# Kernel tuning notes

Hardware: AMD Instinct MI355X
Metric: run time of the kernel (lower is better)

Reference implementation:

```python
import jax, jax.numpy as jnp
import numpy as np

N_NODES = 50000
N_EDGES = 800000
D_IN, H, D_OUT = 128, 128, 64


def setup_inputs() -> dict:
    key = jax.random.key(0)
    ks = jax.random.split(key, 8)
    x = jax.random.normal(ks[0], (N_NODES, D_IN), dtype=jnp.float32)
    edge_index = jax.random.randint(ks[1], (2, N_EDGES), 0, N_NODES, dtype=jnp.int64)
    s = 0.05
    return {
        "x": x,
        "edge_index": edge_index,
        # PyG Linear weights are [out, in]; y = x @ W.T + b
        "W_rel1": jax.random.normal(ks[2], (H, D_IN), dtype=jnp.float32) * s,
        "W_root1": jax.random.normal(ks[3], (H, D_IN), dtype=jnp.float32) * s,
        "b1": jax.random.normal(ks[4], (H,), dtype=jnp.float32) * s,
        "W_rel2": jax.random.normal(ks[5], (D_OUT, H), dtype=jnp.float32) * s,
        "W_root2": jax.random.normal(ks[6], (D_OUT, H), dtype=jnp.float32) * s,
        "b2": jax.random.normal(ks[7], (D_OUT,), dtype=jnp.float32) * s,
    }


def graph_conv(x, src, dst, W_rel, W_root, b):
    # sum-aggregate raw neighbor features, then apply linear (equivalent to
    # transforming each message first, but cheaper: one gather + one GEMM).
    agg = jax.ops.segment_sum(x[src], dst, num_segments=N_NODES)  # [N, D]
    return jnp.einsum('nd,hd->nh', agg, W_rel) \
         + jnp.einsum('nd,hd->nh', x, W_root) + b


def reference(x, edge_index, W_rel1, W_root1, b1, W_rel2, W_root2, b2):
    src, dst = edge_index[0], edge_index[1]  # messages flow src -> dst
    t = jax.nn.relu(graph_conv(x, src, dst, W_rel1, W_root1, b1))
    t = graph_conv(t, src, dst, W_rel2, W_root2, b2)
    return t
```

## Files before the change

kernel.cpp:

```cpp
#include <hip/hip_runtime.h>

#define NNODES 50000
#define DIM 128
#define SCAN_CHUNK 4096
#define NSCAN 13
#define PREP_BLOCKS 3200
#define POISON ((int)0xAAAAAAAA)

typedef __attribute__((ext_vector_type(8))) __bf16 bf16x8;
typedef __attribute__((ext_vector_type(4))) float f32x4;

__device__ inline unsigned short f2b(float f) {
    unsigned int u = __float_as_uint(f);
    u += 0x7fffu + ((u >> 16) & 1u);
    return (unsigned short)(u >> 16);
}
__device__ inline float blo(unsigned int u) { return __uint_as_float(u << 16); }
__device__ inline float bhi(unsigned int u) { return __uint_as_float(u & 0xffff0000u); }
__device__ inline unsigned int pack2(float a, float b) {
    return (unsigned int)f2b(a) | ((unsigned int)f2b(b) << 16);
}

__global__ __launch_bounds__(256) void k_prep(
    const float* __restrict__ x, unsigned short* __restrict__ xb, int n4,
    const float* __restrict__ Wa1, const float* __restrict__ Wb1,
    const float* __restrict__ Wa2, const float* __restrict__ Wb2,
    unsigned short* __restrict__ wa1, unsigned short* __restrict__ wb1,
    unsigned short* __restrict__ wa2, unsigned short* __restrict__ wb2,
    const int* __restrict__ dst, int* __restrict__ counts,
    int* __restrict__ rank, int n_edges)
{
    const int gid = blockIdx.x * 256 + threadIdx.x;

    const int i1 = blockIdx.x * 512 + threadIdx.x;
    const int i2 = i1 + 256;
    const bool ok1 = i1 < n4, ok2 = i2 < n4;
    float4 v1, v2;
    if (ok1) v1 = reinterpret_cast<const float4*>(x)[i1];
    if (ok2) v2 = reinterpret_cast<const float4*>(x)[i2];

    if (gid < n_edges) rank[gid] = atomicAdd(&counts[dst[gid]], 1);

    if (gid < 16384) { wa1[gid] = f2b(Wa1[gid]); wb1[gid] = f2b(Wb1[gid]); }
    if (gid < 8192)  { wa2[gid] = f2b(Wa2[gid]); wb2[gid] = f2b(Wb2[gid]); }

    if (ok1) {
        uint2 o;
        o.x = pack2(v1.x, v1.y);
        o.y = pack2(v1.z, v1.w);
        reinterpret_cast<uint2*>(xb)[i1] = o;
    }
    if (ok2) {
        uint2 o;
        o.x = pack2(v2.x, v2.y);
        o.y = pack2(v2.z, v2.w);
        reinterpret_cast<uint2*>(xb)[i2] = o;
    }
}

__global__ __launch_bounds__(1024) void k_scan_local(
    const int* __restrict__ counts, int* __restrict__ rowptr,
    int* __restrict__ bsum, int n)
{
    __shared__ int wsum[16];
    const int lane = threadIdx.x & 63;
    const int wid = threadIdx.x >> 6;
    int i = blockIdx.x * SCAN_CHUNK + threadIdx.x * 4;
    int4 v = make_int4(0, 0, 0, 0);
    if (i + 3 < n) {
        v = *reinterpret_cast<const int4*>(counts + i);
        v.x -= POISON; v.y -= POISON; v.z -= POISON; v.w -= POISON;
    } else {
        if (i + 0 < n) v.x = counts[i + 0] - POISON;
        if (i + 1 < n) v.y = counts[i + 1] - POISON;
        if (i + 2 < n) v.z = counts[i + 2] - POISON;
    }
    int tot = v.x + v.y + v.z + v.w;
    int s = tot;
#pragma unroll
    for (int off = 1; off < 64; off <<= 1) {
        int t = __shfl_up(s, off);
        if (lane >= off) s += t;
    }
    if (lane == 63) wsum[wid] = s;
    __syncthreads();
    if (wid == 0 && lane < 16) {
        int ws = wsum[lane];
#pragma unroll
        for (int off = 1; off < 16; off <<= 1) {
            int t = __shfl_up(ws, off);
            if (lane >= off) ws += t;
        }
        wsum[lane] = ws;
    }
    __syncthreads();
    int prefix = ((wid > 0) ? wsum[wid - 1] : 0) + (s - tot);
    int4 o;
    o.x = prefix;
    o.y = prefix + v.x;
    o.z = o.y + v.y;
    o.w = o.z + v.z;
    if (i + 3 <= n) {
        *reinterpret_cast<int4*>(rowptr + i) = o;
    } else {
        if (i + 0 <= n) rowptr[i + 0] = o.x;
        if (i + 1 <= n) rowptr[i + 1] = o.y;
        if (i + 2 <= n) rowptr[i + 2] = o.z;
    }
    if (threadIdx.x == 1023) bsum[blockIdx.x] = wsum[15];
}

__device__ inline void build_prefix_lds(const int* __restrict__ bsum, int* pre) {
    if (threadIdx.x < 16) {
        int off = 0;
#pragma unroll 1
        for (int j = 0; j < NSCAN && j < (int)threadIdx.x; ++j) off += bsum[j];
        pre[threadIdx.x] = off;
    }
    __syncthreads();
}

__global__ __launch_bounds__(256) void k_place(
    const int* __restrict__ src, const int* __restrict__ dst,
    const int* __restrict__ rank, const int* __restrict__ rowptr,
    const int* __restrict__ bsum, int* __restrict__ srcs_sorted, int n_edges)
{
    __shared__ int pre[16];
    build_prefix_lds(bsum, pre);
    int e = (blockIdx.x * 256 + threadIdx.x) * 8;
    if (e + 7 < n_edges) {
        int4 s4a = *reinterpret_cast<const int4*>(src + e);
        int4 s4b = *reinterpret_cast<const int4*>(src + e + 4);
        int4 d4a = *reinterpret_cast<const int4*>(dst + e);
        int4 d4b = *reinterpret_cast<const int4*>(dst + e + 4);
        int4 r4a = *reinterpret_cast<const int4*>(rank + e);
        int4 r4b = *reinterpret_cast<const int4*>(rank + e + 4);
        srcs_sorted[rowptr[d4a.x] + pre[d4a.x >> 12] + r4a.x - POISON] = s4a.x;
        srcs_sorted[rowptr[d4a.y] + pre[d4a.y >> 12] + r4a.y - POISON] = s4a.y;
        srcs_sorted[rowptr[d4a.z] + pre[d4a.z >> 12] + r4a.z - POISON] = s4a.z;
        srcs_sorted[rowptr[d4a.w] + pre[d4a.w >> 12] + r4a.w - POISON] = s4a.w;
        srcs_sorted[rowptr[d4b.x] + pre[d4b.x >> 12] + r4b.x - POISON] = s4b.x;
        srcs_sorted[rowptr[d4b.y] + pre[d4b.y >> 12] + r4b.y - POISON] = s4b.y;
        srcs_sorted[rowptr[d4b.z] + pre[d4b.z >> 12] + r4b.z - POISON] = s4b.z;
        srcs_sorted[rowptr[d4b.w] + pre[d4b.w >> 12] + r4b.w - POISON] = s4b.w;
    } else {
        for (; e < n_edges; ++e) {
            int d = dst[e];
            srcs_sorted[rowptr[d] + pre[d >> 12] + rank[e] - POISON] = src[e];
        }
    }
}

__global__ __launch_bounds__(256) void k_gather_sum(
    const unsigned short* __restrict__ xb, const int* __restrict__ rowptr,
    const int* __restrict__ bsum, const int* __restrict__ srcs,
    unsigned short* __restrict__ aggb)
{
    __shared__ int pre[16];
    build_prefix_lds(bsum, pre);
    int node = blockIdx.x * 16 + (threadIdx.x >> 4);
    if (node >= NNODES) return;
    int seg = threadIdx.x & 15;
    int beg = rowptr[node] + pre[node >> 12];
    int end = rowptr[node + 1] + pre[(node + 1) >> 12];
    float acc[8];
#pragma unroll
    for (int i = 0; i < 8; ++i) acc[i] = 0.f;
    int e = beg;
#pragma unroll 1
    for (; e + 7 < end; e += 8) {
        uint4 v[8];
#pragma unroll
        for (int u = 0; u < 8; ++u) {
            int s = srcs[e + u];
            v[u] = *reinterpret_cast<const uint4*>(xb + (size_t)s * DIM + seg * 8);
        }
#pragma unroll
        for (int u = 0; u < 8; ++u) {
            acc[0] += blo(v[u].x); acc[1] += bhi(v[u].x);
            acc[2] += blo(v[u].y); acc[3] += bhi(v[u].y);
            acc[4] += blo(v[u].z); acc[5] += bhi(v[u].z);
            acc[6] += blo(v[u].w); acc[7] += bhi(v[u].w);
        }
    }
#pragma unroll 1
    for (; e + 1 < end; e += 2) {
        int s0 = srcs[e], s1 = srcs[e + 1];
        uint4 v0 = *reinterpret_cast<const uint4*>(xb + (size_t)s0 * DIM + seg * 8);
        uint4 v1 = *reinterpret_cast<const uint4*>(xb + (size_t)s1 * DIM + seg * 8);
        acc[0] += blo(v0.x) + blo(v1.x); acc[1] += bhi(v0.x) + bhi(v1.x);
        acc[2] += blo(v0.y) + blo(v1.y); acc[3] += bhi(v0.y) + bhi(v1.y);
        acc[4] += blo(v0.z) + blo(v1.z); acc[5] += bhi(v0.z) + bhi(v1.z);
        acc[6] += blo(v0.w) + blo(v1.w); acc[7] += bhi(v0.w) + bhi(v1.w);
    }
    if (e < end) {
        int s0 = srcs[e];
        uint4 v = *reinterpret_cast<const uint4*>(xb + (size_t)s0 * DIM + seg * 8);
        acc[0] += blo(v.x); acc[1] += bhi(v.x);
        acc[2] += blo(v.y); acc[3] += bhi(v.y);
        acc[4] += blo(v.z); acc[5] += bhi(v.z);
        acc[6] += blo(v.w); acc[7] += bhi(v.w);
    }
    uint4 o;
    o.x = pack2(acc[0], acc[1]);
    o.y = pack2(acc[2], acc[3]);
    o.z = pack2(acc[4], acc[5]);
    o.w = pack2(acc[6], acc[7]);
    *reinterpret_cast<uint4*>(aggb + (size_t)node * DIM + seg * 8) = o;
}

template <int BN, bool RELU, bool OUTBF16>
__global__ __launch_bounds__(256) void k_gemm_direct(
    const unsigned short* __restrict__ Ab,
    const unsigned short* __restrict__ Bb,
    const unsigned short* __restrict__ Wa,
    const unsigned short* __restrict__ Wb,
    const float* __restrict__ bias, void* __restrict__ Cout, int n_nodes)
{
    constexpr int NT = BN / 16;
    const int tid = threadIdx.x;
    const int wave = tid >> 6;
    const int lane = tid & 63;
    const int quad = lane >> 4;
    const int l16 = lane & 15;
    const int n0 = blockIdx.x * 64;
    const int arow = n0 + wave * 16 + l16;
    const bool ok = arow < n_nodes;

    f32x4 acc[NT];
#pragma unroll
    for (int nt = 0; nt < NT; ++nt) {
        f32x4 z = {0.f, 0.f, 0.f, 0.f};
        acc[nt] = z;
    }

#pragma unroll 1
    for (int kk = 0; kk < 4; ++kk) {
        const unsigned short* __restrict__ Asrc = (kk < 2) ? Ab : Bb;
        const unsigned short* __restrict__ Wsrc = (kk < 2) ? Wa : Wb;
        const int ko = (kk & 1) * 64;
        bf16x8 a0 = {}, a1 = {};
        if (ok) {
            a0 = *reinterpret_cast<const bf16x8*>(
                Asrc + (size_t)arow * DIM + ko + quad * 8);
            a1 = *reinterpret_cast<const bf16x8*>(
                Asrc + (size_t)arow * DIM + ko + 32 + quad * 8);
        }
#pragma unroll
        for (int nt = 0; nt < NT; ++nt) {
            bf16x8 b = *reinterpret_cast<const bf16x8*>(
                Wsrc + (size_t)(nt * 16 + l16) * DIM + ko + quad * 8);
            acc[nt] = __builtin_amdgcn_mfma_f32_16x16x32_bf16(a0, b, acc[nt], 0, 0, 0);
        }
#pragma unroll
        for (int nt = 0; nt < NT; ++nt) {
            bf16x8 b = *reinterpret_cast<const bf16x8*>(
                Wsrc + (size_t)(nt * 16 + l16) * DIM + ko + 32 + quad * 8);
            acc[nt] = __builtin_amdgcn_mfma_f32_16x16x32_bf16(a1, b, acc[nt], 0, 0, 0);
        }
    }

#pragma unroll
    for (int nt = 0; nt < NT; ++nt) {
        int col = nt * 16 + l16;
        float bv = bias[col];
#pragma unroll
        for (int reg = 0; reg < 4; ++reg) {
            int row = n0 + wave * 16 + quad * 4 + reg;
            if (row >= n_nodes) continue;
            float v = acc[nt][reg] + bv;
            if (RELU) v = fmaxf(v, 0.f);
            if (OUTBF16)
                ((unsigned short*)Cout)[(size_t)row * BN + col] = f2b(v);
            else
                ((float*)Cout)[(size_t)row * BN + col] = v;
        }
    }
}

extern "C" void kernel_launch(void* const* d_in, const int* in_sizes, int n_in,
                              void* d_out, int out_size, void* d_ws, size_t ws_size,
                              hipStream_t stream) {
    const float* x       = (const float*)d_in[0];
    const int*   ei      = (const int*)d_in[1];
    const float* W_rel1  = (const float*)d_in[2];
    const float* W_root1 = (const float*)d_in[3];
    const float* b1      = (const float*)d_in[4];
    const float* W_rel2  = (const float*)d_in[5];
    const float* W_root2 = (const float*)d_in[6];
    const float* b2      = (const float*)d_in[7];

    const int n_edges = in_sizes[1] / 2;
    const int* src = ei;
    const int* dst = ei + n_edges;

    const size_t NELEM = (size_t)NNODES * DIM;
    unsigned short* xb   = (unsigned short*)d_ws;
    unsigned short* aggb = xb + NELEM;
    unsigned short* tb   = aggb + NELEM;
    unsigned short* wa1  = tb + NELEM;
    unsigned short* wb1  = wa1 + 16384;
    unsigned short* wa2  = wb1 + 16384;
    unsigned short* wb2  = wa2 + 8192;
    int* counts = (int*)(wb2 + 8192);
    int* rowptr = counts + NNODES;
    int* bsum   = rowptr + (NNODES + 4);
    int* rank   = bsum + 20;
    int* srcs   = rank + n_edges;

    float* out = (float*)d_out;

    const int n4 = NNODES * DIM / 4;
    const int pblocks = (n_edges + 2047) / 2048;
    const int gblocks = (NNODES + 15) / 16;
    const int gemm_blocks = (NNODES + 63) / 64;
    const int sblocks = NSCAN;

    k_prep<<<PREP_BLOCKS, 256, 0, stream>>>(
        x, xb, n4, W_rel1, W_root1, W_rel2, W_root2,
        wa1, wb1, wa2, wb2, dst, counts, rank, n_edges);

    k_scan_local<<<sblocks, 1024, 0, stream>>>(counts, rowptr, bsum, NNODES);
    k_place<<<pblocks, 256, 0, stream>>>(src, dst, rank, rowptr, bsum, srcs, n_edges);

    k_gather_sum<<<gblocks, 256, 0, stream>>>(xb, rowptr, bsum, srcs, aggb);
    k_gemm_direct<128, true, true><<<gemm_blocks, 256, 0, stream>>>(
        aggb, xb, wa1, wb1, b1, tb, NNODES);

    k_gather_sum<<<gblocks, 256, 0, stream>>>(tb, rowptr, bsum, srcs, aggb);
    k_gemm_direct<64, false, false><<<gemm_blocks, 256, 0, stream>>>(
        aggb, tb, wa2, wb2, b2, out, NNODES);
}
```

Measured before the change: 257.2 us.

## Fuse neighbor gather-sum with GEMM via LDS and shrink edge indices to 16-bit

The separate gather-sum and GEMM kernels are merged into one kernel per layer. Each 32-node block accumulates its neighbor sums into an LDS tile and then runs bf16 MFMA over that tile plus the root features, so the aggregated matrix is never written to or read back from global memory. Separately, the per-edge rank and the sorted source-index arrays are stored as 16-bit values, which halves index traffic in the place and gather steps. The 16-bit storage only works while node ids and per-node degrees stay below 65536. The GEMM tile also shrinks to 32 rows, with waves split across output columns, which could lower the arithmetic efficiency of the GEMM stage.

```diff
diff --git a/kernel.cpp b/kernel.cpp
--- a/kernel.cpp
+++ b/kernel.cpp
@@ -28,7 +28,7 @@
     unsigned short* __restrict__ wa1, unsigned short* __restrict__ wb1,
     unsigned short* __restrict__ wa2, unsigned short* __restrict__ wb2,
     const int* __restrict__ dst, int* __restrict__ counts,
-    int* __restrict__ rank, int n_edges)
+    unsigned short* __restrict__ rank, int n_edges)
 {
     const int gid = blockIdx.x * 256 + threadIdx.x;
 
@@ -39,7 +39,8 @@
     if (ok1) v1 = reinterpret_cast<const float4*>(x)[i1];
     if (ok2) v2 = reinterpret_cast<const float4*>(x)[i2];
 
-    if (gid < n_edges) rank[gid] = atomicAdd(&counts[dst[gid]], 1);
+    if (gid < n_edges)
+        rank[gid] = (unsigned short)(atomicAdd(&counts[dst[gid]], 1) - POISON);
 
     if (gid < 16384) { wa1[gid] = f2b(Wa1[gid]); wb1[gid] = f2b(Wb1[gid]); }
     if (gid < 8192)  { wa2[gid] = f2b(Wa2[gid]); wb2[gid] = f2b(Wb2[gid]); }
@@ -122,8 +123,9 @@
 
 __global__ __launch_bounds__(256) void k_place(
     const int* __restrict__ src, const int* __restrict__ dst,
-    const int* __restrict__ rank, const int* __restrict__ rowptr,
-    const int* __restrict__ bsum, int* __restrict__ srcs_sorted, int n_edges)
+    const unsigned short* __restrict__ rank, const int* __restrict__ rowptr,
+    const int* __restrict__ bsum, unsigned short* __restrict__ srcs_sorted,
+    int n_edges)
 {
     __shared__ int pre[16];
     build_prefix_lds(bsum, pre);
@@ -133,99 +135,105 @@
         int4 s4b = *reinterpret_cast<const int4*>(src + e + 4);
         int4 d4a = *reinterpret_cast<const int4*>(dst + e);
         int4 d4b = *reinterpret_cast<const int4*>(dst + e + 4);
-        int4 r4a = *reinterpret_cast<const int4*>(rank + e);
-        int4 r4b = *reinterpret_cast<const int4*>(rank + e + 4);
-        srcs_sorted[rowptr[d4a.x] + pre[d4a.x >> 12] + r4a.x - POISON] = s4a.x;
-        srcs_sorted[rowptr[d4a.y] + pre[d4a.y >> 12] + r4a.y - POISON] = s4a.y;
-        srcs_sorted[rowptr[d4a.z] + pre[d4a.z >> 12] + r4a.z - POISON] = s4a.z;
-        srcs_sorted[rowptr[d4a.w] + pre[d4a.w >> 12] + r4a.w - POISON] = s4a.w;
-        srcs_sorted[rowptr[d4b.x] + pre[d4b.x >> 12] + r4b.x - POISON] = s4b.x;
-        srcs_sorted[rowptr[d4b.y] + pre[d4b.y >> 12] + r4b.y - POISON] = s4b.y;
-        srcs_sorted[rowptr[d4b.z] + pre[d4b.z >> 12] + r4b.z - POISON] = s4b.z;
-        srcs_sorted[rowptr[d4b.w] + pre[d4b.w >> 12] + r4b.w - POISON] = s4b.w;
+        uint4 r8 = *reinterpret_cast<const uint4*>(rank + e);
+        srcs_sorted[rowptr[d4a.x] + pre[d4a.x >> 12] + (int)(r8.x & 0xffffu)] = (unsigned short)s4a.x;
+        srcs_sorted[rowptr[d4a.y] + pre[d4a.y >> 12] + (int)(r8.x >> 16)]     = (unsigned short)s4a.y;
+        srcs_sorted[rowptr[d4a.z] + pre[d4a.z >> 12] + (int)(r8.y & 0xffffu)] = (unsigned short)s4a.z;
+        srcs_sorted[rowptr[d4a.w] + pre[d4a.w >> 12] + (int)(r8.y >> 16)]     = (unsigned short)s4a.w;
+        srcs_sorted[rowptr[d4b.x] + pre[d4b.x >> 12] + (int)(r8.z & 0xffffu)] = (unsigned short)s4b.x;
+        srcs_sorted[rowptr[d4b.y] + pre[d4b.y >> 12] + (int)(r8.z >> 16)]     = (unsigned short)s4b.y;
+        srcs_sorted[rowptr[d4b.z] + pre[d4b.z >> 12] + (int)(r8.w & 0xffffu)] = (unsigned short)s4b.z;
+        srcs_sorted[rowptr[d4b.w] + pre[d4b.w >> 12] + (int)(r8.w >> 16)]     = (unsigned short)s4b.w;
     } else {
         for (; e < n_edges; ++e) {
             int d = dst[e];
-            srcs_sorted[rowptr[d] + pre[d >> 12] + rank[e] - POISON] = src[e];
-        }
-    }
-}
-
-__global__ __launch_bounds__(256) void k_gather_sum(
-    const unsigned short* __restrict__ xb, const int* __restrict__ rowptr,
-    const int* __restrict__ bsum, const int* __restrict__ srcs,
-    unsigned short* __restrict__ aggb)
+            srcs_sorted[rowptr[d] + pre[d >> 12] + (int)rank[e]] = (unsigned short)src[e];
+        }
+    }
+}
+
+template <int BN, bool RELU, bool OUTBF16>
+__global__ __launch_bounds__(256) void k_fused(
+    const unsigned short* __restrict__ F,
+    const int* __restrict__ rowptr, const int* __restrict__ bsum,
+    const unsigned short* __restrict__ srcs,
+    const unsigned short* __restrict__ Wrel,
+    const unsigned short* __restrict__ Wroot,
+    const float* __restrict__ bias, void* __restrict__ Cout, int n_nodes)
 {
     __shared__ int pre[16];
+    __shared__ __align__(16) unsigned short agg[32][136];
     build_prefix_lds(bsum, pre);
-    int node = blockIdx.x * 16 + (threadIdx.x >> 4);
-    if (node >= NNODES) return;
-    int seg = threadIdx.x & 15;
-    int beg = rowptr[node] + pre[node >> 12];
-    int end = rowptr[node + 1] + pre[(node + 1) >> 12];
-    float acc[8];
-#pragma unroll
-    for (int i = 0; i < 8; ++i) acc[i] = 0.f;
-    int e = beg;
-#pragma unroll 1
-    for (; e + 7 < end; e += 8) {
-        uint4 v[8];
-#pragma unroll
-        for (int u = 0; u < 8; ++u) {
-            int s = srcs[e + u];
-            v[u] = *reinterpret_cast<const uint4*>(xb + (size_t)s * DIM + seg * 8);
-        }
-#pragma unroll
-        for (int u = 0; u < 8; ++u) {
-            acc[0] += blo(v[u].x); acc[1] += bhi(v[u].x);
-            acc[2] += blo(v[u].y); acc[3] += bhi(v[u].y);
-            acc[4] += blo(v[u].z); acc[5] += bhi(v[u].z);
-            acc[6] += blo(v[u].w); acc[7] += bhi(v[u].w);
-        }
-    }
-#pragma unroll 1
-    for (; e + 1 < end; e += 2) {
-        int s0 = srcs[e], s1 = srcs[e + 1];
-        uint4 v0 = *reinterpret_cast<const uint4*>(xb + (size_t)s0 * DIM + seg * 8);
-        uint4 v1 = *reinterpret_cast<const uint4*>(xb + (size_t)s1 * DIM + seg * 8);
-        acc[0] += blo(v0.x) + blo(v1.x); acc[1] += bhi(v0.x) + bhi(v1.x);
-        acc[2] += blo(v0.y) + blo(v1.y); acc[3] += bhi(v0.y) + bhi(v1.y);
-        acc[4] += blo(v0.z) + blo(v1.z); acc[5] += bhi(v0.z) + bhi(v1.z);
-        acc[6] += blo(v0.w) + blo(v1.w); acc[7] += bhi(v0.w) + bhi(v1.w);
-    }
-    if (e < end) {
-        int s0 = srcs[e];
-        uint4 v = *reinterpret_cast<const uint4*>(xb + (size_t)s0 * DIM + seg * 8);
-        acc[0] += blo(v.x); acc[1] += bhi(v.x);
-        acc[2] += blo(v.y); acc[3] += bhi(v.y);
-        acc[4] += blo(v.z); acc[5] += bhi(v.z);
-        acc[6] += blo(v.w); acc[7] += bhi(v.w);
-    }
-    uint4 o;
-    o.x = pack2(acc[0], acc[1]);
-    o.y = pack2(acc[2], acc[3]);
-    o.z = pack2(acc[4], acc[5]);
-    o.w = pack2(acc[6], acc[7]);
-    *reinterpret_cast<uint4*>(aggb + (size_t)node * DIM + seg * 8) = o;
-}
-
-template <int BN, bool RELU, bool OUTBF16>
-__global__ __launch_bounds__(256) void k_gemm_direct(
-    const unsigned short* __restrict__ Ab,
-    const unsigned short* __restrict__ Bb,
-    const unsigned short* __restrict__ Wa,
-    const unsigned short* __restrict__ Wb,
-    const float* __restrict__ bias, void* __restrict__ Cout, int n_nodes)
-{
-    constexpr int NT = BN / 16;
+
     const int tid = threadIdx.x;
+    const int n0 = blockIdx.x * 32;
+
+#pragma unroll 1
+    for (int pass = 0; pass < 2; ++pass) {
+        const int nl = pass * 16 + (tid >> 4);
+        const int node = n0 + nl;
+        const int seg = tid & 15;
+        if (node < n_nodes) {
+            const int beg = rowptr[node] + pre[node >> 12];
+            const int end = rowptr[node + 1] + pre[(node + 1) >> 12];
+            float acc[8];
+#pragma unroll
+            for (int i = 0; i < 8; ++i) acc[i] = 0.f;
+            int e = beg;
+#pragma unroll 1
+            for (; e + 7 < end; e += 8) {
+                uint4 v[8];
+#pragma unroll
+                for (int u = 0; u < 8; ++u) {
+                    int s = srcs[e + u];
+                    v[u] = *reinterpret_cast<const uint4*>(F + (size_t)s * DIM + seg * 8);
+                }
+#pragma unroll
+                for (int u = 0; u < 8; ++u) {
+                    acc[0] += blo(v[u].x); acc[1] += bhi(v[u].x);
+                    acc[2] += blo(v[u].y); acc[3] += bhi(v[u].y);
+                    acc[4] += blo(v[u].z); acc[5] += bhi(v[u].z);
+                    acc[6] += blo(v[u].w); acc[7] += bhi(v[u].w);
+                }
+            }
+#pragma unroll 1
+            for (; e + 1 < end; e += 2) {
+                int s0 = srcs[e], s1 = srcs[e + 1];
+                uint4 v0 = *reinterpret_cast<const uint4*>(F + (size_t)s0 * DIM + seg * 8);
+                uint4 v1 = *reinterpret_cast<const uint4*>(F + (size_t)s1 * DIM + seg * 8);
+                acc[0] += blo(v0.x) + blo(v1.x); acc[1] += bhi(v0.x) + bhi(v1.x);
+                acc[2] += blo(v0.y) + blo(v1.y); acc[3] += bhi(v0.y) + bhi(v1.y);
+                acc[4] += blo(v0.z) + blo(v1.z); acc[5] += bhi(v0.z) + bhi(v1.z);
+                acc[6] += blo(v0.w) + blo(v1.w); acc[7] += bhi(v0.w) + bhi(v1.w);
+            }
+            if (e < end) {
+                int s0 = srcs[e];
+                uint4 v = *reinterpret_cast<const uint4*>(F + (size_t)s0 * DIM + seg * 8);
+                acc[0] += blo(v.x); acc[1] += bhi(v.x);
+                acc[2] += blo(v.y); acc[3] += bhi(v.y);
+                acc[4] += blo(v.z); acc[5] += bhi(v.z);
+                acc[6] += blo(v.w); acc[7] += bhi(v.w);
+            }
+            uint4 o;
+            o.x = pack2(acc[0], acc[1]);
+            o.y = pack2(acc[2], acc[3]);
+            o.z = pack2(acc[4], acc[5]);
+            o.w = pack2(acc[6], acc[7]);
+            *reinterpret_cast<uint4*>(&agg[nl][seg * 8]) = o;
+        }
+    }
+    __syncthreads();
+
+    constexpr int NT = BN / 32;
     const int wave = tid >> 6;
     const int lane = tid & 63;
     const int quad = lane >> 4;
     const int l16 = lane & 15;
-    const int n0 = blockIdx.x * 64;
-    const int arow = n0 + wave * 16 + l16;
-    const bool ok = arow < n_nodes;
+    const int wr = wave >> 1;
+    const int wc = wave & 1;
+    const int rl = wr * 16 + l16;
+    const int grow = n0 + rl;
+    const bool ok = grow < n_nodes;
 
     f32x4 acc[NT];
 #pragma unroll
@@ -236,37 +244,39 @@
 
 #pragma unroll 1
     for (int kk = 0; kk < 4; ++kk) {
-        const unsigned short* __restrict__ Asrc = (kk < 2) ? Ab : Bb;
-        const unsigned short* __restrict__ Wsrc = (kk < 2) ? Wa : Wb;
         const int ko = (kk & 1) * 64;
         bf16x8 a0 = {}, a1 = {};
-        if (ok) {
+        if (kk < 2) {
+            a0 = *reinterpret_cast<const bf16x8*>(&agg[rl][ko + quad * 8]);
+            a1 = *reinterpret_cast<const bf16x8*>(&agg[rl][ko + 32 + quad * 8]);
+        } else if (ok) {
             a0 = *reinterpret_cast<const bf16x8*>(
-                Asrc + (size_t)arow * DIM + ko + quad * 8);
+                F + (size_t)grow * DIM + ko + quad * 8);
             a1 = *reinterpret_cast<const bf16x8*>(
-                Asrc + (size_t)arow * DIM + ko + 32 + quad * 8);
-        }
+                F + (size_t)grow * DIM + ko + 32 + quad * 8);
+        }
+        const unsigned short* __restrict__ W = (kk < 2) ? Wrel : Wroot;
 #pragma unroll
         for (int nt = 0; nt < NT; ++nt) {
             bf16x8 b = *reinterpret_cast<const bf16x8*>(
-                Wsrc + (size_t)(nt * 16 + l16) * DIM + ko + quad * 8);
+                W + (size_t)(wc * (BN / 2) + nt * 16 + l16) * DIM + ko + quad * 8);
             acc[nt] = __builtin_amdgcn_mfma_f32_16x16x32_bf16(a0, b, acc[nt], 0, 0, 0);
         }
 #pragma unroll
         for (int nt = 0; nt < NT; ++nt) {
             bf16x8 b = *reinterpret_cast<const bf16x8*>(
-                Wsrc + (size_t)(nt * 16 + l16) * DIM + ko + 32 + quad * 8);
+                W + (size_t)(wc * (BN / 2) + nt * 16 + l16) * DIM + ko + 32 + quad * 8);
             acc[nt] = __builtin_amdgcn_mfma_f32_16x16x32_bf16(a1, b, acc[nt], 0, 0, 0);
         }
     }
 
 #pragma unroll
     for (int nt = 0; nt < NT; ++nt) {
-        int col = nt * 16 + l16;
-        float bv = bias[col];
+        const int col = wc * (BN / 2) + nt * 16 + l16;
+        const float bv = bias[col];
 #pragma unroll
         for (int reg = 0; reg < 4; ++reg) {
-            int row = n0 + wave * 16 + quad * 4 + reg;
+            const int row = n0 + wr * 16 + quad * 4 + reg;
             if (row >= n_nodes) continue;
             float v = acc[nt][reg] + bv;
             if (RELU) v = fmaxf(v, 0.f);
@@ -296,8 +306,7 @@
 
     const size_t NELEM = (size_t)NNODES * DIM;
     unsigned short* xb   = (unsigned short*)d_ws;
-    unsigned short* aggb = xb + NELEM;
-    unsigned short* tb   = aggb + NELEM;
+    unsigned short* tb   = xb + NELEM;
     unsigned short* wa1  = tb + NELEM;
     unsigned short* wb1  = wa1 + 16384;
     unsigned short* wa2  = wb1 + 16384;
@@ -305,29 +314,26 @@
     int* counts = (int*)(wb2 + 8192);
     int* rowptr = counts + NNODES;
     int* bsum   = rowptr + (NNODES + 4);
-    int* rank   = bsum + 20;
-    int* srcs   = rank + n_edges;
+    unsigned short* rank16 = (unsigned short*)(bsum + 20);
+    unsigned short* srcs16 = rank16 + n_edges;
 
     float* out = (float*)d_out;
 
     const int n4 = NNODES * DIM / 4;
     const int pblocks = (n_edges + 2047) / 2048;
-    const int gblocks = (NNODES + 15) / 16;
-    const int gemm_blocks = (NNODES + 63) / 64;
+    const int fblocks = (NNODES + 31) / 32;
     const int sblocks = NSCAN;
 
     k_prep<<<PREP_BLOCKS, 256, 0, stream>>>(
         x, xb, n4, W_rel1, W_root1, W_rel2, W_root2,
-        wa1, wb1, wa2, wb2, dst, counts, rank, n_edges);
+        wa1, wb1, wa2, wb2, dst, counts, rank16, n_edges);
 
     k_scan_local<<<sblocks, 1024, 0, stream>>>(counts, rowptr, bsum, NNODES);
-    k_place<<<pblocks, 256, 0, stream>>>(src, dst, rank, rowptr, bsum, srcs, n_edges);
-
-    k_gather_sum<<<gblocks, 256, 0, stream>>>(xb, rowptr, bsum, srcs, aggb);
-    k_gemm_direct<128, true, true><<<gemm_blocks, 256, 0, stream>>>(
-        aggb, xb, wa1, wb1, b1, tb, NNODES);
-
-    k_gather_sum<<<gblocks, 256, 0, stream>>>(tb, rowptr, bsum, srcs, aggb);
-    k_gemm_direct<64, false, false><<<gemm_blocks, 256, 0, stream>>>(
-        aggb, tb, wa2, wb2, b2, out, NNODES);
-}
+    k_place<<<pblocks, 256, 0, stream>>>(src, dst, rank16, rowptr, bsum, srcs16, n_edges);
+
+    k_fused<128, true, true><<<fblocks, 256, 0, stream>>>(
+        xb, rowptr, bsum, srcs16, wa1, wb1, b1, tb, NNODES);
+
+    k_fused<64, false, false><<<fblocks, 256, 0, stream>>>(
+        tb, rowptr, bsum, srcs16, wa2, wb2, b2, out, NNODES);
+}
```

New measurement: 256.1 us. No clear change (-0.4%).
